# Performance work log

Hardware: AMD Instinct MI355X
Metric: run time of the kernel (lower is better)

## Reference

```python
import jax, jax.numpy as jnp
import numpy as np

B, S, E, H = 4, 2048, 1024, 16
D = E // H  # head_dim = 64


def setup_inputs() -> dict:
    key = jax.random.key(0)
    ks = jax.random.split(key, 9)
    s = 1.0 / np.sqrt(E)
    return {
        "x": jax.random.normal(ks[0], (B, S, E), dtype=jnp.float32),
        "mask": jnp.ones((B, S), dtype=jnp.int32),
        "Wq": jax.random.uniform(ks[1], (E, E), jnp.float32, -s, s),
        "bq": jnp.zeros((E,), jnp.float32),
        "Wk": jax.random.uniform(ks[2], (E, E), jnp.float32, -s, s),
        "bk": jnp.zeros((E,), jnp.float32),
        "Wv": jax.random.uniform(ks[3], (E, E), jnp.float32, -s, s),
        "bv": jnp.zeros((E,), jnp.float32),
        "Wo": jax.random.uniform(ks[4], (E, E), jnp.float32, -s, s),
        "bo": jnp.zeros((E,), jnp.float32),
    }


def reference(x, mask, Wq, bq, Wk, bk, Wv, bv, Wo, bo):
    # projections: weights stored as (in, out)
    q = x @ Wq + bq  # [B,S,E]
    k = x @ Wk + bk
    v = x @ Wv + bv
    # split heads: b s (h d) -> b h s d
    q = q.reshape(B, S, H, D).transpose(0, 2, 1, 3)
    k = k.reshape(B, S, H, D).transpose(0, 2, 1, 3)
    v = v.reshape(B, S, H, D).transpose(0, 2, 1, 3)
    scale = 1.0 / np.sqrt(D).astype(np.float32)
    dot = jnp.einsum('bhsd,bhtd->bhst', q, k) * scale  # [B,H,S,S]
    # key padding mask: 1 = valid, 0 = masked
    neg_inf = jnp.asarray(-jnp.inf, dot.dtype)
    dot = jnp.where(mask[:, None, None, :] == 0, neg_inf, dot)
    attn = jax.nn.softmax(dot, axis=-1)
    o = jnp.einsum('bhst,bhtd->bhsd', attn, v)  # [B,H,S,D]
    o = o.transpose(0, 2, 1, 3).reshape(B, S, E)  # merge heads
    return o @ Wo + bo
```

## Files before the change

### kernel.cpp

```cpp
#include <hip/hip_runtime.h>

#define Bc 4
#define Sc 2048
#define Ec 1024
#define Hc 16
#define Dc 64
#define BSc 8192
#define KVB 64

typedef short bf16x8 __attribute__((ext_vector_type(8)));
typedef float f32x4 __attribute__((ext_vector_type(4)));
typedef unsigned short u16;
typedef unsigned long long u64;

__device__ __forceinline__ u16 f2bf(float f){
  unsigned u = __builtin_bit_cast(unsigned, f);
  u += 0x7FFFu + ((u >> 16) & 1u);
  return (u16)(u >> 16);
}
__device__ __forceinline__ void gll16(const void* g, void* l){
  __builtin_amdgcn_global_load_lds((const __attribute__((address_space(1))) void*)g,
                                   (__attribute__((address_space(3))) void*)l, 16, 0, 0);
}
__device__ __forceinline__ float exp2_s(float x){
#if __has_builtin(__builtin_amdgcn_exp2f)
  return __builtin_amdgcn_exp2f(x);
#else
  float r;
  asm volatile("v_exp_f32 %0, %1\n\ts_nop 1" : "=v"(r) : "v"(x));
  return r;
#endif
}
__device__ __forceinline__ unsigned cvtpk(float a, float b){
  unsigned r;
  asm volatile("v_cvt_pk_bf16_f32 %0, %1, %2\n\ts_nop 1" : "=v"(r) : "v"(a), "v"(b));
  return r;
}

__global__ void cvt_x_kernel(const float* __restrict__ x, u16* __restrict__ xb, int n){
  int i = (blockIdx.x * 256 + threadIdx.x) * 4;
  if (i >= n) return;
  float4 v = *(const float4*)(x + i);
  *(ushort4*)(xb+i) = make_ushort4(f2bf(v.x), f2bf(v.y), f2bf(v.z), f2bf(v.w));
}

__global__ void wt_kernel(const float* __restrict__ w0, const float* __restrict__ w1,
                          const float* __restrict__ w2, const float* __restrict__ w3,
                          u16* __restrict__ wt){
  const float* w = blockIdx.z==0 ? w0 : blockIdx.z==1 ? w1 : blockIdx.z==2 ? w2 : w3;
  u16* ho = wt + (size_t)blockIdx.z * Ec * Ec;
  __shared__ float t[32][33];
  int k0 = blockIdx.y * 32, n0 = blockIdx.x * 32;
  int tx = threadIdx.x & 31, ty = threadIdx.x >> 5;
  for (int i = 0; i < 4; ++i){
    int k = ty + i*8;
    t[k][tx] = w[(size_t)(k0+k)*Ec + n0 + tx];
  }
  __syncthreads();
  for (int i = 0; i < 4; ++i){
    int nn = ty + i*8;
    ho[(size_t)(n0+nn)*Ec + k0 + tx] = f2bf(t[tx][nn]);
  }
}

template<int MODE>
__global__ __launch_bounds__(256, 2)
void gemm_bt(const u16* __restrict__ A, const u16* __restrict__ Bt,
             const float* __restrict__ bias, void* __restrict__ outp)
{
  constexpr int K = Ec;
  __shared__ alignas(16) u16 As[128*32];
  __shared__ alignas(16) u16 Bs[128*32];
  const int tid = threadIdx.x, lane = tid & 63, w = tid >> 6;
  const int wr = w >> 1, wc = w & 1;
  const int m0 = blockIdx.y * 128, n0 = blockIdx.x * 128;
  const int l15 = lane & 15, kslot = lane >> 4;
  const f32x4 fz = {0.f,0.f,0.f,0.f};
  f32x4 acc[4][4];
  for (int i=0;i<4;++i) for (int j=0;j<4;++j) acc[i][j] = fz;

  const int srow = lane >> 2, sslot = lane & 3;

  for (int k0 = 0; k0 < K; k0 += 32){
    __syncthreads();
    for (int i = 0; i < 2; ++i){
      int c = w*2 + i;
      int row = c*16 + srow;
      int sw = (row ^ (row >> 2)) & 3;
      gll16(A  + (size_t)(m0+row)*K + k0 + ((sslot ^ sw) << 3), As + c*512);
      gll16(Bt + (size_t)(n0+row)*K + k0 + ((sslot ^ sw) << 3), Bs + c*512);
    }
    __syncthreads();
    bf16x8 af[4], bfr[4];
    for (int mi = 0; mi < 4; ++mi){
      int row = wr*64 + mi*16 + l15;
      int sw = (row ^ (row >> 2)) & 3;
      af[mi] = *(const bf16x8*)(As + row*32 + ((kslot ^ sw) << 3));
    }
    for (int ni = 0; ni < 4; ++ni){
      int row = wc*64 + ni*16 + l15;
      int sw = (row ^ (row >> 2)) & 3;
      bfr[ni] = *(const bf16x8*)(Bs + row*32 + ((kslot ^ sw) << 3));
    }
    for (int mi = 0; mi < 4; ++mi)
      for (int ni = 0; ni < 4; ++ni)
        acc[mi][ni] = __builtin_amdgcn_mfma_f32_16x16x32_bf16(af[mi], bfr[ni], acc[mi][ni], 0, 0, 0);
  }

  for (int mi = 0; mi < 4; ++mi){
    for (int ni = 0; ni < 4; ++ni){
      int col = n0 + wc*64 + ni*16 + l15;
      int row0 = m0 + wr*64 + mi*16 + kslot*4;
      float bi = bias[col];
      if (MODE == 2){
        int bb = row0 >> 11, s0 = row0 & 2047;
        int hh = col >> 6, dd = col & 63;
        ushort4 pk = make_ushort4(f2bf(acc[mi][ni][0]+bi), f2bf(acc[mi][ni][1]+bi),
                                  f2bf(acc[mi][ni][2]+bi), f2bf(acc[mi][ni][3]+bi));
        *(ushort4*)((u16*)outp + ((size_t)(bb*Hc+hh)*Dc + dd)*Sc + s0) = pk;
      } else {
        for (int j = 0; j < 4; ++j){
          float v = acc[mi][ni][j] + bi;
          int row = row0 + j;
          if (MODE == 0 || MODE == 1){
            float vv = (MODE == 0) ? v * 0.18033688f : v;
            int bb = row >> 11, ss = row & 2047;
            int hh = col >> 6, dd = col & 63;
            ((u16*)outp)[((size_t)(bb*Hc+hh)*Sc + ss)*Dc + dd] = f2bf(vv);
          } else {
            ((float*)outp)[(size_t)row*Ec + col] = v;
          }
        }
      }
    }
  }
}

__global__ __launch_bounds__(256, 2)
void attn_kernel(const u16* __restrict__ qb, const u16* __restrict__ kb,
                 const u16* __restrict__ vt, const int* __restrict__ mask,
                 u16* __restrict__ ob)
{
  __shared__ alignas(16) u16 Ks[2][KVB*Dc];
  __shared__ alignas(16) u16 Vs[2][Dc*KVB];
  const int tid = threadIdx.x, lane = tid & 63, w = tid >> 6;
  const int l15 = lane & 15, ks = lane >> 4;
  const int wg = ((blockIdx.x & 7) << 7) | (blockIdx.x >> 3);
  const int bh = wg >> 4, qblk = wg & 15;
  const int b = bh >> 4, h = bh & 15;
  const int q0 = qblk*128 + w*32;

  const u16* Q  = qb + (size_t)bh*Sc*Dc;
  const u16* Kg = kb + (size_t)bh*Sc*Dc;
  const u16* Vg = vt + (size_t)bh*Dc*Sc;
  const int* mpb = mask + b*Sc;

  int koff[2], voff[2];
#pragma unroll
  for (int i = 0; i < 2; ++i){
    int S = (w*2+i)*64 + lane;
    int row = S >> 3, s = S & 7;
    koff[i] = row*Dc + ((s ^ (row & 7)) << 3);
    voff[i] = row*Sc + ((s ^ (row & 7)) << 3);
  }
  const int Xl = (l15 & 7) << 4;

  bf16x8 qf[2][2];
#pragma unroll
  for (int qa = 0; qa < 2; ++qa)
#pragma unroll
    for (int kd = 0; kd < 2; ++kd)
      qf[qa][kd] = *(const bf16x8*)(Q + (size_t)(q0 + qa*16 + l15)*Dc + kd*32 + ks*8);

  bf16x8 onesb;
#pragma unroll
  for (int j = 0; j < 8; ++j) onesb[j] = (short)0x3F80;

  const f32x4 fz = {0.f,0.f,0.f,0.f};
  f32x4 o[2][4];
#pragma unroll
  for (int qa = 0; qa < 2; ++qa)
#pragma unroll
    for (int db = 0; db < 4; ++db) o[qa][db] = fz;
  float m[2] = {-3e38f, -3e38f}, runl[2] = {0.f, 0.f};

#pragma unroll
  for (int i = 0; i < 2; ++i){
    gll16(Kg + koff[i], &Ks[0][(w*2+i)*512]);
    gll16(Vg + voff[i], &Vs[0][(w*2+i)*512]);
  }

  const int NT = Sc / KVB;
  int cur = 0;
  for (int t = 0; t < NT; ++t){
    asm volatile("s_waitcnt vmcnt(0)" ::: "memory");
    __syncthreads();
    if (t + 1 < NT){
      const u16* kg = Kg + (size_t)(t+1)*(KVB*Dc);
      const u16* vg = Vg + (size_t)(t+1)*KVB;
#pragma unroll
      for (int i = 0; i < 2; ++i){
        gll16(kg + koff[i], &Ks[cur^1][(w*2+i)*512]);
        gll16(vg + voff[i], &Vs[cur^1][(w*2+i)*512]);
      }
    }
    const char* Ksb = (const char*)&Ks[cur][0];
    const char* Vsb = (const char*)&Vs[cur][0];

    f32x4 sc[4][2];
#pragma unroll
    for (int nb = 0; nb < 4; ++nb){
      bf16x8 kf0 = *(const bf16x8*)(Ksb + nb*2048 + l15*128 + (((0*4+ks) << 4) ^ Xl));
      bf16x8 kf1 = *(const bf16x8*)(Ksb + nb*2048 + l15*128 + (((1*4+ks) << 4) ^ Xl));
#pragma unroll
      for (int qa = 0; qa < 2; ++qa){
        sc[nb][qa] = __builtin_amdgcn_mfma_f32_16x16x32_bf16(kf0, qf[qa][0], fz, 0,0,0);
        sc[nb][qa] = __builtin_amdgcn_mfma_f32_16x16x32_bf16(kf1, qf[qa][1], sc[nb][qa], 0,0,0);
      }
    }
    const int* mp = mpb + t*KVB;
    int mv = mp[lane];
    if (!__all(mv != 0)){
#pragma unroll
      for (int nb = 0; nb < 4; ++nb)
#pragma unroll
        for (int r = 0; r < 4; ++r){
          float bi = mp[nb*16 + ks*4 + r] ? 0.f : -3e38f;
          sc[nb][0][r] += bi;
          sc[nb][1][r] += bi;
        }
    }
    float tmax[2];
#pragma unroll
    for (int qa = 0; qa < 2; ++qa){
      f32x4 mx4;
#pragma unroll
      for (int r = 0; r < 4; ++r)
        mx4[r] = fmaxf(fmaxf(sc[0][qa][r], sc[1][qa][r]),
                       fmaxf(sc[2][qa][r], sc[3][qa][r]));
      float tv = fmaxf(fmaxf(mx4[0], mx4[1]), fmaxf(mx4[2], mx4[3]));
      tv = fmaxf(tv, __shfl_xor(tv, 16, 64));
      tv = fmaxf(tv, __shfl_xor(tv, 32, 64));
      tmax[qa] = tv;
    }
    bool need = (t == 0) ||
                !__all((tmax[0] <= m[0] + 8.f) && (tmax[1] <= m[1] + 8.f));
    if (need){
#pragma unroll
      for (int qa = 0; qa < 2; ++qa){
        float nm = fmaxf(m[qa], tmax[qa]);
        float al = exp2_s(m[qa] - nm);
        m[qa] = nm;
        runl[qa] *= al;
#pragma unroll
        for (int db = 0; db < 4; ++db)
#pragma unroll
          for (int r = 0; r < 4; ++r)
            o[qa][db][r] *= al;
      }
    }
#pragma unroll
    for (int nb = 0; nb < 4; ++nb)
#pragma unroll
      for (int qa = 0; qa < 2; ++qa)
#pragma unroll
        for (int r = 0; r < 4; ++r)
          sc[nb][qa][r] = exp2_s(sc[nb][qa][r] - m[qa]);

    f32x4 accl[2] = {fz, fz};
#pragma unroll
    for (int kt = 0; kt < 2; ++kt){
      bf16x8 pb[2];
#pragma unroll
      for (int qa = 0; qa < 2; ++qa){
        union { bf16x8 v; unsigned u[4]; } pu;
        pu.u[0] = cvtpk(sc[2*kt  ][qa][0], sc[2*kt  ][qa][1]);
        pu.u[1] = cvtpk(sc[2*kt  ][qa][2], sc[2*kt  ][qa][3]);
        pu.u[2] = cvtpk(sc[2*kt+1][qa][0], sc[2*kt+1][qa][1]);
        pu.u[3] = cvtpk(sc[2*kt+1][qa][2], sc[2*kt+1][qa][3]);
        pb[qa] = pu.v;
      }
      accl[0] = __builtin_amdgcn_mfma_f32_16x16x32_bf16(onesb, pb[0], accl[0], 0,0,0);
      accl[1] = __builtin_amdgcn_mfma_f32_16x16x32_bf16(onesb, pb[1], accl[1], 0,0,0);
#pragma unroll
      for (int db = 0; db < 4; ++db){
        union { bf16x8 v; u64 q[2]; } vu;
        const int g0 = kt*4 + (ks >> 1);
        const int base = db*2048 + l15*128 + (ks & 1)*8;
        vu.q[0] = *(const u64*)(Vsb + base + (((g0    ) << 4) ^ Xl));
        vu.q[1] = *(const u64*)(Vsb + base + (((g0 + 2) << 4) ^ Xl));
#pragma unroll
        for (int qa = 0; qa < 2; ++qa)
          o[qa][db] = __builtin_amdgcn_mfma_f32_16x16x32_bf16(vu.v, pb[qa], o[qa][db], 0,0,0);
      }
    }
    runl[0] += accl[0][0];
    runl[1] += accl[1][0];
    cur ^= 1;
  }
#pragma unroll
  for (int qa = 0; qa < 2; ++qa){
    float inv = __builtin_amdgcn_rcpf(fmaxf(runl[qa], 1e-35f));
    u16* orow = ob + ((size_t)(b*Sc + q0 + qa*16 + l15))*Ec + h*Dc + ks*4;
#pragma unroll
    for (int db = 0; db < 4; ++db){
      ushort4 pk = make_ushort4(f2bf(o[qa][db][0]*inv), f2bf(o[qa][db][1]*inv),
                                f2bf(o[qa][db][2]*inv), f2bf(o[qa][db][3]*inv));
      *(ushort4*)(orow + db*16) = pk;
    }
  }
}

extern "C" void kernel_launch(void* const* d_in, const int* in_sizes, int n_in,
                              void* d_out, int out_size, void* d_ws, size_t ws_size,
                              hipStream_t stream) {
  const float* x  = (const float*)d_in[0];
  const int* mask = (const int*)d_in[1];
  const float* Wq = (const float*)d_in[2];
  const float* bq = (const float*)d_in[3];
  const float* Wk = (const float*)d_in[4];
  const float* bk = (const float*)d_in[5];
  const float* Wv = (const float*)d_in[6];
  const float* bv = (const float*)d_in[7];
  const float* Wo = (const float*)d_in[8];
  const float* bo = (const float*)d_in[9];
  float* out = (float*)d_out;

  u16* ws   = (u16*)d_ws;
  u16* x_bf = ws;
  u16* w_t  = x_bf + (size_t)BSc*Ec;
  u16* q_bf = w_t  + (size_t)4*Ec*Ec;
  u16* k_bf = q_bf + (size_t)BSc*Ec;
  u16* v_t  = k_bf + (size_t)BSc*Ec;
  u16* o_bf = v_t  + (size_t)BSc*Ec;

  cvt_x_kernel<<<BSc*Ec/1024, 256, 0, stream>>>(x, x_bf, BSc*Ec);
  wt_kernel<<<dim3(32,32,4), 256, 0, stream>>>(Wq, Wk, Wv, Wo, w_t);

  const size_t WSZ = (size_t)Ec*Ec;
  gemm_bt<0><<<dim3(8,64), 256, 0, stream>>>(x_bf, w_t+0*WSZ, bq, q_bf);
  gemm_bt<1><<<dim3(8,64), 256, 0, stream>>>(x_bf, w_t+1*WSZ, bk, k_bf);
  gemm_bt<2><<<dim3(8,64), 256, 0, stream>>>(x_bf, w_t+2*WSZ, bv, v_t);

  attn_kernel<<<dim3(1024), 256, 0, stream>>>(q_bf, k_bf, v_t, mask, o_bf);

  gemm_bt<3><<<dim3(8,64), 256, 0, stream>>>(o_bf, w_t+3*WSZ, bo, out);
}
```

Before: 224.7 us.

## Fuse QKV projections into one launch and hoist mask check in attention

Merges the three Q/K/V projection GEMMs into a single kernel with a 24x64 grid, where each block picks its weight slice and epilogue from its column index. The aim is to cut launch count and fill the GPU better with a larger grid. The attention kernel now scans the whole key mask once up front, so the per-tile mask load and wave vote run only when some key is masked. It also defers the cross-lane max shuffles to the rescale path. This adds a small per-block prologue read of the mask and a runtime branch on `which` inside the fused GEMM epilogue.

Measured after the change: 204.3 us. 1.1x faster.

```diff
diff --git a/kernel.cpp b/kernel.cpp
--- a/kernel.cpp
+++ b/kernel.cpp
@@ -63,10 +63,85 @@
   }
 }
 
-template<int MODE>
 __global__ __launch_bounds__(256, 2)
-void gemm_bt(const u16* __restrict__ A, const u16* __restrict__ Bt,
-             const float* __restrict__ bias, void* __restrict__ outp)
+void gemm_qkv(const u16* __restrict__ A, const u16* __restrict__ Wt,
+              const float* __restrict__ bq, const float* __restrict__ bk,
+              const float* __restrict__ bv,
+              u16* __restrict__ qout, u16* __restrict__ kout, u16* __restrict__ vout)
+{
+  constexpr int K = Ec;
+  __shared__ alignas(16) u16 As[128*32];
+  __shared__ alignas(16) u16 Bs[128*32];
+  const int tid = threadIdx.x, lane = tid & 63, w = tid >> 6;
+  const int wr = w >> 1, wc = w & 1;
+  const int m0 = blockIdx.y * 128;
+  const int n0g = blockIdx.x * 128;
+  const int which = n0g >> 10;
+  const int n0 = n0g & 1023;
+  const u16* Bt = Wt + (size_t)which * Ec * Ec;
+  const float* bias = which == 0 ? bq : which == 1 ? bk : bv;
+  const int l15 = lane & 15, kslot = lane >> 4;
+  const f32x4 fz = {0.f,0.f,0.f,0.f};
+  f32x4 acc[4][4];
+  for (int i=0;i<4;++i) for (int j=0;j<4;++j) acc[i][j] = fz;
+
+  const int srow = lane >> 2, sslot = lane & 3;
+
+  for (int k0 = 0; k0 < K; k0 += 32){
+    __syncthreads();
+    for (int i = 0; i < 2; ++i){
+      int c = w*2 + i;
+      int row = c*16 + srow;
+      int sw = (row ^ (row >> 2)) & 3;
+      gll16(A  + (size_t)(m0+row)*K + k0 + ((sslot ^ sw) << 3), As + c*512);
+      gll16(Bt + (size_t)(n0+row)*K + k0 + ((sslot ^ sw) << 3), Bs + c*512);
+    }
+    __syncthreads();
+    bf16x8 af[4], bfr[4];
+    for (int mi = 0; mi < 4; ++mi){
+      int row = wr*64 + mi*16 + l15;
+      int sw = (row ^ (row >> 2)) & 3;
+      af[mi] = *(const bf16x8*)(As + row*32 + ((kslot ^ sw) << 3));
+    }
+    for (int ni = 0; ni < 4; ++ni){
+      int row = wc*64 + ni*16 + l15;
+      int sw = (row ^ (row >> 2)) & 3;
+      bfr[ni] = *(const bf16x8*)(Bs + row*32 + ((kslot ^ sw) << 3));
+    }
+    for (int mi = 0; mi < 4; ++mi)
+      for (int ni = 0; ni < 4; ++ni)
+        acc[mi][ni] = __builtin_amdgcn_mfma_f32_16x16x32_bf16(af[mi], bfr[ni], acc[mi][ni], 0, 0, 0);
+  }
+
+  for (int mi = 0; mi < 4; ++mi){
+    for (int ni = 0; ni < 4; ++ni){
+      int col = n0 + wc*64 + ni*16 + l15;
+      int row0 = m0 + wr*64 + mi*16 + kslot*4;
+      float bi = bias[col];
+      if (which == 2){
+        int bb = row0 >> 11, s0 = row0 & 2047;
+        int hh = col >> 6, dd = col & 63;
+        ushort4 pk = make_ushort4(f2bf(acc[mi][ni][0]+bi), f2bf(acc[mi][ni][1]+bi),
+                                  f2bf(acc[mi][ni][2]+bi), f2bf(acc[mi][ni][3]+bi));
+        *(ushort4*)(vout + ((size_t)(bb*Hc+hh)*Dc + dd)*Sc + s0) = pk;
+      } else {
+        u16* dst = which == 0 ? qout : kout;
+        for (int j = 0; j < 4; ++j){
+          float v = acc[mi][ni][j] + bi;
+          int row = row0 + j;
+          float vv = (which == 0) ? v * 0.18033688f : v;
+          int bb = row >> 11, ss = row & 2047;
+          int hh = col >> 6, dd = col & 63;
+          dst[((size_t)(bb*Hc+hh)*Sc + ss)*Dc + dd] = f2bf(vv);
+        }
+      }
+    }
+  }
+}
+
+__global__ __launch_bounds__(256, 2)
+void gemm_out(const u16* __restrict__ A, const u16* __restrict__ Bt,
+              const float* __restrict__ bias, float* __restrict__ outp)
 {
   constexpr int K = Ec;
   __shared__ alignas(16) u16 As[128*32];
@@ -112,26 +187,8 @@
       int col = n0 + wc*64 + ni*16 + l15;
       int row0 = m0 + wr*64 + mi*16 + kslot*4;
       float bi = bias[col];
-      if (MODE == 2){
-        int bb = row0 >> 11, s0 = row0 & 2047;
-        int hh = col >> 6, dd = col & 63;
-        ushort4 pk = make_ushort4(f2bf(acc[mi][ni][0]+bi), f2bf(acc[mi][ni][1]+bi),
-                                  f2bf(acc[mi][ni][2]+bi), f2bf(acc[mi][ni][3]+bi));
-        *(ushort4*)((u16*)outp + ((size_t)(bb*Hc+hh)*Dc + dd)*Sc + s0) = pk;
-      } else {
-        for (int j = 0; j < 4; ++j){
-          float v = acc[mi][ni][j] + bi;
-          int row = row0 + j;
-          if (MODE == 0 || MODE == 1){
-            float vv = (MODE == 0) ? v * 0.18033688f : v;
-            int bb = row >> 11, ss = row & 2047;
-            int hh = col >> 6, dd = col & 63;
-            ((u16*)outp)[((size_t)(bb*Hc+hh)*Sc + ss)*Dc + dd] = f2bf(vv);
-          } else {
-            ((float*)outp)[(size_t)row*Ec + col] = v;
-          }
-        }
-      }
+      for (int j = 0; j < 4; ++j)
+        outp[(size_t)(row0+j)*Ec + col] = acc[mi][ni][j] + bi;
     }
   }
 }
@@ -155,6 +212,17 @@
   const u16* Vg = vt + (size_t)bh*Dc*Sc;
   const int* mpb = mask + b*Sc;
 
+  int nzl = 1;
+  {
+    const int4* mv4 = (const int4*)mpb;
+#pragma unroll
+    for (int i = 0; i < 8; ++i){
+      int4 v = mv4[i*64 + lane];
+      nzl &= (v.x && v.y && v.z && v.w) ? 1 : 0;
+    }
+  }
+  const bool allvalid = __all(nzl);
+
   int koff[2], voff[2];
 #pragma unroll
   for (int i = 0; i < 2; ++i){
@@ -218,9 +286,8 @@
         sc[nb][qa] = __builtin_amdgcn_mfma_f32_16x16x32_bf16(kf1, qf[qa][1], sc[nb][qa], 0,0,0);
       }
     }
-    const int* mp = mpb + t*KVB;
-    int mv = mp[lane];
-    if (!__all(mv != 0)){
+    if (!allvalid){
+      const int* mp = mpb + t*KVB;
 #pragma unroll
       for (int nb = 0; nb < 4; ++nb)
 #pragma unroll
@@ -230,7 +297,7 @@
           sc[nb][1][r] += bi;
         }
     }
-    float tmax[2];
+    float pmax[2];
 #pragma unroll
     for (int qa = 0; qa < 2; ++qa){
       f32x4 mx4;
@@ -238,17 +305,16 @@
       for (int r = 0; r < 4; ++r)
         mx4[r] = fmaxf(fmaxf(sc[0][qa][r], sc[1][qa][r]),
                        fmaxf(sc[2][qa][r], sc[3][qa][r]));
-      float tv = fmaxf(fmaxf(mx4[0], mx4[1]), fmaxf(mx4[2], mx4[3]));
-      tv = fmaxf(tv, __shfl_xor(tv, 16, 64));
-      tv = fmaxf(tv, __shfl_xor(tv, 32, 64));
-      tmax[qa] = tv;
-    }
-    bool need = (t == 0) ||
-                !__all((tmax[0] <= m[0] + 8.f) && (tmax[1] <= m[1] + 8.f));
-    if (need){
+      pmax[qa] = fmaxf(fmaxf(mx4[0], mx4[1]), fmaxf(mx4[2], mx4[3]));
+    }
+    int ok = (t > 0) && (pmax[0] <= m[0] + 8.f) && (pmax[1] <= m[1] + 8.f);
+    if (!__all(ok)){
 #pragma unroll
       for (int qa = 0; qa < 2; ++qa){
-        float nm = fmaxf(m[qa], tmax[qa]);
+        float tv = pmax[qa];
+        tv = fmaxf(tv, __shfl_xor(tv, 16, 64));
+        tv = fmaxf(tv, __shfl_xor(tv, 32, 64));
+        float nm = fmaxf(m[qa], tv);
         float al = exp2_s(m[qa] - nm);
         m[qa] = nm;
         runl[qa] *= al;
@@ -338,11 +404,9 @@
   wt_kernel<<<dim3(32,32,4), 256, 0, stream>>>(Wq, Wk, Wv, Wo, w_t);
 
   const size_t WSZ = (size_t)Ec*Ec;
-  gemm_bt<0><<<dim3(8,64), 256, 0, stream>>>(x_bf, w_t+0*WSZ, bq, q_bf);
-  gemm_bt<1><<<dim3(8,64), 256, 0, stream>>>(x_bf, w_t+1*WSZ, bk, k_bf);
-  gemm_bt<2><<<dim3(8,64), 256, 0, stream>>>(x_bf, w_t+2*WSZ, bv, v_t);
+  gemm_qkv<<<dim3(24,64), 256, 0, stream>>>(x_bf, w_t, bq, bk, bv, q_bf, k_bf, v_t);
 
   attn_kernel<<<dim3(1024), 256, 0, stream>>>(q_bf, k_bf, v_t, mask, o_bf);
 
-  gemm_bt<3><<<dim3(8,64), 256, 0, stream>>>(o_bf, w_t+3*WSZ, bo, out);
-}
+  gemm_out<<<dim3(8,64), 256, 0, stream>>>(o_bf, w_t+3*WSZ, bo, out);
+}
```
